# Performance work log

Hardware: AMD Instinct MI355X
Metric: run time of the kernel (lower is better)

The kernel has to match this reference:

```python
import jax, jax.numpy as jnp
import numpy as np

PARENTS = np.array([-1, 0, 1, 1, 1])
NECK_CHAIN = np.array([1, 0])  # neck joint (1) up to root (0)
B, V, F, J, S, E = 512, 5023, 9976, 5, 100, 50
L_STAT, L_DYN, L_FULL, N_BUCKET = 51, 17, 68, 79


def rodrigues(rvec):
    """Axis-angle [N,3] -> rotation matrices [N,3,3]."""
    angle = jnp.linalg.norm(rvec + 1e-8, axis=-1, keepdims=True)  # [N,1]
    axis = rvec / angle
    s = jnp.sin(angle)[..., None]
    c = jnp.cos(angle)[..., None]
    rx, ry, rz = axis[:, 0], axis[:, 1], axis[:, 2]
    z = jnp.zeros_like(rx)
    K = jnp.stack([z, -rz, ry, rz, z, -rx, -ry, rx, z], axis=-1).reshape(-1, 3, 3)
    I = jnp.eye(3, dtype=rvec.dtype)
    return I + s * K + (1.0 - c) * (K @ K)


def verts2lmk(vertices, faces, lmk_faces_idx, lmk_bary):
    lmk_faces = faces[lmk_faces_idx]                               # [B,L,3]
    lmk_verts = jax.vmap(lambda v, f: v[f])(vertices, lmk_faces)   # [B,L,3verts,3xyz]
    return jnp.einsum('blfc,blf->blc', lmk_verts, lmk_bary)


def setup_inputs() -> dict:
    key = jax.random.key(0)
    ks = jax.random.split(key, 16)
    shape_params = jax.random.normal(ks[0], (B, S), jnp.float32)
    expression_params = jax.random.normal(ks[1], (B, E), jnp.float32)
    pose_params = 0.2 * jax.random.normal(ks[2], (B, 6), jnp.float32)
    eye_pose_params = 0.1 * jax.random.normal(ks[3], (B, 6), jnp.float32)
    v_template = jax.random.normal(ks[4], (V, 3), jnp.float32) * 0.1
    shapedirs = jax.random.normal(ks[5], (V, 3, S + E), jnp.float32) * 0.01
    posedirs = jax.random.normal(ks[6], ((J - 1) * 9, V * 3), jnp.float32) * 0.01
    jr = jax.random.uniform(ks[7], (J, V), jnp.float32)
    J_regressor = jr / jnp.sum(jr, axis=1, keepdims=True)
    lbs_weights = jax.nn.softmax(jax.random.normal(ks[8], (V, J), jnp.float32), axis=-1)
    faces = jax.random.randint(ks[9], (F, 3), 0, V)
    lmk_faces_idx = jax.random.randint(ks[10], (L_STAT,), 0, F)
    lb = jax.random.uniform(ks[11], (L_STAT, 3), jnp.float32) + 1e-3
    lmk_bary_coords = lb / jnp.sum(lb, axis=-1, keepdims=True)
    dynamic_lmk_faces_idx = jax.random.randint(ks[12], (N_BUCKET, L_DYN), 0, F)
    db = jax.random.uniform(ks[13], (N_BUCKET, L_DYN, 3), jnp.float32) + 1e-3
    dynamic_lmk_bary_coords = db / jnp.sum(db, axis=-1, keepdims=True)
    full_lmk_faces_idx = jax.random.randint(ks[14], (L_FULL,), 0, F)
    fb = jax.random.uniform(ks[15], (L_FULL, 3), jnp.float32) + 1e-3
    full_lmk_bary_coords = fb / jnp.sum(fb, axis=-1, keepdims=True)
    return {
        'shape_params': shape_params, 'expression_params': expression_params,
        'pose_params': pose_params, 'eye_pose_params': eye_pose_params,
        'v_template': v_template, 'shapedirs': shapedirs, 'posedirs': posedirs,
        'J_regressor': J_regressor, 'lbs_weights': lbs_weights, 'faces': faces,
        'lmk_faces_idx': lmk_faces_idx, 'lmk_bary_coords': lmk_bary_coords,
        'dynamic_lmk_faces_idx': dynamic_lmk_faces_idx,
        'dynamic_lmk_bary_coords': dynamic_lmk_bary_coords,
        'full_lmk_faces_idx': full_lmk_faces_idx,
        'full_lmk_bary_coords': full_lmk_bary_coords,
    }


def reference(shape_params, expression_params, pose_params, eye_pose_params,
              v_template, shapedirs, posedirs, J_regressor, lbs_weights, faces,
              lmk_faces_idx, lmk_bary_coords, dynamic_lmk_faces_idx,
              dynamic_lmk_bary_coords, full_lmk_faces_idx, full_lmk_bary_coords):
    b = shape_params.shape[0]
    nv = v_template.shape[0]
    dt = shape_params.dtype
    betas = jnp.concatenate([shape_params, expression_params], axis=1)          # [B,150]
    neck = jnp.zeros((b, 3), dtype=dt)
    full_pose = jnp.concatenate(
        [pose_params[:, :3], neck, pose_params[:, 3:], eye_pose_params], axis=1)  # [B,15]
    # shape + expression blendshapes
    v_shaped = v_template[None] + jnp.einsum('bl,vcl->bvc', betas, shapedirs)   # [B,V,3]
    joints = jnp.einsum('jv,bvc->bjc', J_regressor, v_shaped)                   # [B,5,3]
    rot_mats = rodrigues(full_pose.reshape(-1, 3)).reshape(b, J, 3, 3)          # [B,5,3,3]
    I3 = jnp.eye(3, dtype=dt)
    pose_feature = (rot_mats[:, 1:] - I3).reshape(b, -1)                        # [B,36]
    v_posed = v_shaped + (pose_feature @ posedirs).reshape(b, nv, 3)
    # kinematic chain -> global joint transforms
    rel_J = joints.at[:, 1:].add(-joints[:, PARENTS[1:]])
    tm = jnp.zeros((b, J, 4, 4), dtype=dt)
    tm = tm.at[:, :, :3, :3].set(rot_mats).at[:, :, :3, 3].set(rel_J).at[:, :, 3, 3].set(1.0)
    chain = [tm[:, 0]]
    for i in range(1, J):
        chain.append(chain[PARENTS[i]] @ tm[:, i])
    A = jnp.stack(chain, axis=1)                                                # [B,5,4,4]
    Rj = jnp.einsum('bjmn,bjn->bjm', A[:, :, :3, :3], joints)
    A_rel = A.at[:, :, :3, 3].add(-Rj)
    # per-vertex skinning
    T = jnp.einsum('vj,bjmn->bvmn', lbs_weights, A_rel)                         # [B,V,4,4]
    vertices = jnp.einsum('bvmn,bvn->bvm', T[:, :, :3, :3], v_posed) + T[:, :, :3, 3]
    # dynamic contour landmark selection from neck kin-chain relative rotation
    aa = full_pose.reshape(b, J, 3)[:, NECK_CHAIN]                              # [B,2,3]
    rc = rodrigues(aa.reshape(-1, 3)).reshape(b, len(NECK_CHAIN), 3, 3)
    rel_rot = jnp.broadcast_to(I3, (b, 3, 3))
    for idx in range(len(NECK_CHAIN)):
        rel_rot = rc[:, idx] @ rel_rot
    sy = jnp.sqrt(rel_rot[:, 0, 0] ** 2 + rel_rot[:, 1, 0] ** 2)
    y_deg = jnp.arctan2(-rel_rot[:, 2, 0], sy) * (180.0 / np.pi)
    y_rot = jnp.round(jnp.minimum(y_deg, 39.0)).astype(jnp.int32)
    neg_mask = y_rot < 0
    big_neg = y_rot < -39
    neg_vals = jnp.where(big_neg, 78, 39 - y_rot)
    y_rot = jnp.where(neg_mask, neg_vals, y_rot)                                # [B] in [0,79)
    dyn_faces = dynamic_lmk_faces_idx[y_rot]                                    # [B,17]
    dyn_bary = dynamic_lmk_bary_coords[y_rot]                                   # [B,17,3]
    lf = jnp.concatenate([dyn_faces, jnp.broadcast_to(lmk_faces_idx[None], (b, lmk_faces_idx.shape[0]))], axis=1)
    lb = jnp.concatenate([dyn_bary, jnp.broadcast_to(lmk_bary_coords[None], (b,) + lmk_bary_coords.shape)], axis=1)
    landmarks2d = verts2lmk(vertices, faces, lf, lb)
    ff = jnp.broadcast_to(full_lmk_faces_idx[None], (b, full_lmk_faces_idx.shape[0]))
    fb = jnp.broadcast_to(full_lmk_bary_coords[None], (b,) + full_lmk_bary_coords.shape)
    landmarks3d = verts2lmk(vertices, faces, ff, fb)
    return (vertices, landmarks2d, landmarks3d)
```

## Files before the change

kernel.cpp:

```cpp
#include <hip/hip_runtime.h>
#include <cstddef>
#include <cstdint>

#define cB   512
#define cV   5023
#define cS   100
#define cE   50
#define cJ   5
#define cLD  17
#define cLF  68

#define cV3    15069
#define cNPAD  15072
#define cKPAD  192

#define OUT_V  ((size_t)cB * cV * 3)
#define OUT_L  ((size_t)cB * cLF * 3)

#define WS_BTN   ((size_t)0)
#define WS_ATM   (WS_BTN + (size_t)cNPAD * 96)
#define WS_JS2   (WS_ATM + (size_t)cB * 96)
#define WS_AREL  (WS_JS2 + 2432)
#define WS_PF    (WS_AREL + (size_t)cB * 60)
#define WS_YROT  (WS_PF + (size_t)cB * 36)

typedef __attribute__((ext_vector_type(8))) short short8;
typedef __attribute__((ext_vector_type(4))) float f32x4;

__device__ __forceinline__ unsigned short f2bf(float x) {
  unsigned int u = __float_as_uint(x);
  u = (u + 0x7fffu + ((u >> 16) & 1u)) >> 16;
  return (unsigned short)u;
}

__device__ __forceinline__ void rodrigues9(float rx, float ry, float rz, float* R) {
  float a0 = rx + 1e-8f, a1 = ry + 1e-8f, a2 = rz + 1e-8f;
  float angle = sqrtf(a0 * a0 + a1 * a1 + a2 * a2);
  float inv = 1.0f / angle;
  float x = rx * inv, y = ry * inv, z = rz * inv;
  float s = sinf(angle), c = cosf(angle);
  float t = 1.0f - c;
  float xy = x * y, xz = x * z, yz = y * z;
  R[0] = 1.0f - t * (y * y + z * z);
  R[1] = -s * z + t * xy;
  R[2] =  s * y + t * xz;
  R[3] =  s * z + t * xy;
  R[4] = 1.0f - t * (x * x + z * z);
  R[5] = -s * x + t * yz;
  R[6] = -s * y + t * xz;
  R[7] =  s * x + t * yz;
  R[8] = 1.0f - t * (x * x + y * y);
}

__global__ void k_js(const float* __restrict__ jreg, const float* __restrict__ sd,
                     const float* __restrict__ vt, float* __restrict__ JSpart) {
  int t = threadIdx.x;
  if (t >= 453) return;
  int c = t / 151, l = t - c * 151;
  int v0 = blockIdx.x * 32;
  int v1 = v0 + 32; if (v1 > cV) v1 = cV;
  float acc[5] = {0.f, 0.f, 0.f, 0.f, 0.f};
#pragma unroll 8
  for (int v = v0; v < v1; ++v) {
    float x = (l < 150) ? sd[(size_t)(v * 3 + c) * 150 + l] : vt[v * 3 + c];
#pragma unroll
    for (int j = 0; j < 5; ++j)
      acc[j] = fmaf(jreg[j * cV + v], x, acc[j]);
  }
#pragma unroll
  for (int j = 0; j < 5; ++j)
    JSpart[(size_t)blockIdx.x * 2272 + (j * 3 + c) * 151 + l] = acc[j];
}

__global__ void k_jsred(const float* __restrict__ JSpart, float* __restrict__ JS2) {
  int e = blockIdx.x * 256 + threadIdx.x;
  if (e >= 2265) return;
  float s = 0.f;
#pragma unroll 8
  for (int p = 0; p < 157; ++p)
    s += JSpart[(size_t)p * 2272 + e];
  int jc = e / 151, l = e - jc * 151;
  JS2[l * 16 + jc] = s;
}

__global__ __launch_bounds__(256) void k_batch(
    const float* __restrict__ shp, const float* __restrict__ expr,
    const float* __restrict__ pose, const float* __restrict__ eyep,
    const float* __restrict__ JS2g, float* __restrict__ Arel,
    float* __restrict__ pf, int* __restrict__ yrot) {
  __shared__ float js2[151 * 16];
  __shared__ float sb[64 * 153];
  const int t = threadIdx.x;
  const int b0 = blockIdx.x * 64;
  for (int i = t; i < 151 * 16; i += 256) js2[i] = JS2g[i];
  for (int e = t; e < 6400; e += 256) {
    int bl = e / 100, l = e - bl * 100;
    sb[bl * 153 + l] = shp[(size_t)(b0 + bl) * 100 + l];
  }
  for (int e = t; e < 3200; e += 256) {
    int bl = e / 50, l = e - bl * 50;
    sb[bl * 153 + 100 + l] = expr[(size_t)(b0 + bl) * 50 + l];
  }
  __syncthreads();
  if (t >= 64) return;
  int b = b0 + t;
  float jnt[5][3];
  {
    const f32x4* J4 = (const f32x4*)(js2 + 150 * 16);
    f32x4 A = J4[0], Bq = J4[1], Cq = J4[2], Dq = J4[3];
    jnt[0][0] = A.x;  jnt[0][1] = A.y;  jnt[0][2] = A.z;
    jnt[1][0] = A.w;  jnt[1][1] = Bq.x; jnt[1][2] = Bq.y;
    jnt[2][0] = Bq.z; jnt[2][1] = Bq.w; jnt[2][2] = Cq.x;
    jnt[3][0] = Cq.y; jnt[3][1] = Cq.z; jnt[3][2] = Cq.w;
    jnt[4][0] = Dq.x; jnt[4][1] = Dq.y; jnt[4][2] = Dq.z;
  }
  for (int l = 0; l < 150; ++l) {
    const f32x4* J4 = (const f32x4*)(js2 + l * 16);
    f32x4 A = J4[0], Bq = J4[1], Cq = J4[2], Dq = J4[3];
    float beta = sb[t * 153 + l];
    jnt[0][0] = fmaf(beta, A.x,  jnt[0][0]);
    jnt[0][1] = fmaf(beta, A.y,  jnt[0][1]);
    jnt[0][2] = fmaf(beta, A.z,  jnt[0][2]);
    jnt[1][0] = fmaf(beta, A.w,  jnt[1][0]);
    jnt[1][1] = fmaf(beta, Bq.x, jnt[1][1]);
    jnt[1][2] = fmaf(beta, Bq.y, jnt[1][2]);
    jnt[2][0] = fmaf(beta, Bq.z, jnt[2][0]);
    jnt[2][1] = fmaf(beta, Bq.w, jnt[2][1]);
    jnt[2][2] = fmaf(beta, Cq.x, jnt[2][2]);
    jnt[3][0] = fmaf(beta, Cq.y, jnt[3][0]);
    jnt[3][1] = fmaf(beta, Cq.z, jnt[3][1]);
    jnt[3][2] = fmaf(beta, Cq.w, jnt[3][2]);
    jnt[4][0] = fmaf(beta, Dq.x, jnt[4][0]);
    jnt[4][1] = fmaf(beta, Dq.y, jnt[4][1]);
    jnt[4][2] = fmaf(beta, Dq.z, jnt[4][2]);
  }
  float fp[5][3];
  fp[0][0] = pose[b * 6 + 0]; fp[0][1] = pose[b * 6 + 1]; fp[0][2] = pose[b * 6 + 2];
  fp[1][0] = 0.f; fp[1][1] = 0.f; fp[1][2] = 0.f;
  fp[2][0] = pose[b * 6 + 3]; fp[2][1] = pose[b * 6 + 4]; fp[2][2] = pose[b * 6 + 5];
  fp[3][0] = eyep[b * 6 + 0]; fp[3][1] = eyep[b * 6 + 1]; fp[3][2] = eyep[b * 6 + 2];
  fp[4][0] = eyep[b * 6 + 3]; fp[4][1] = eyep[b * 6 + 4]; fp[4][2] = eyep[b * 6 + 5];
  float R[5][9];
#pragma unroll
  for (int j = 0; j < 5; ++j) rodrigues9(fp[j][0], fp[j][1], fp[j][2], R[j]);
#pragma unroll
  for (int j = 1; j < 5; ++j)
#pragma unroll
    for (int r = 0; r < 9; ++r) {
      float id = (r == 0 || r == 4 || r == 8) ? 1.f : 0.f;
      pf[b * 36 + (j - 1) * 9 + r] = R[j][r] - id;
    }
  float rel[5][3];
#pragma unroll
  for (int c = 0; c < 3; ++c) {
    rel[0][c] = jnt[0][c];
    rel[1][c] = jnt[1][c] - jnt[0][c];
    rel[2][c] = jnt[2][c] - jnt[1][c];
    rel[3][c] = jnt[3][c] - jnt[1][c];
    rel[4][c] = jnt[4][c] - jnt[1][c];
  }
  float GR[5][9], Gt[5][3];
#pragma unroll
  for (int r = 0; r < 9; ++r) GR[0][r] = R[0][r];
#pragma unroll
  for (int c = 0; c < 3; ++c) Gt[0][c] = rel[0][c];
  const int par[5] = {0, 0, 1, 1, 1};
#pragma unroll
  for (int j = 1; j < 5; ++j) {
    int p = par[j];
#pragma unroll
    for (int r = 0; r < 3; ++r) {
#pragma unroll
      for (int cc = 0; cc < 3; ++cc)
        GR[j][r * 3 + cc] = GR[p][r * 3 + 0] * R[j][0 + cc] +
                            GR[p][r * 3 + 1] * R[j][3 + cc] +
                            GR[p][r * 3 + 2] * R[j][6 + cc];
      Gt[j][r] = Gt[p][r] + GR[p][r * 3 + 0] * rel[j][0] +
                            GR[p][r * 3 + 1] * rel[j][1] +
                            GR[p][r * 3 + 2] * rel[j][2];
    }
  }
#pragma unroll
  for (int j = 0; j < 5; ++j)
#pragma unroll
    for (int r = 0; r < 3; ++r) {
      float tj = Gt[j][r] - (GR[j][r * 3 + 0] * jnt[j][0] +
                             GR[j][r * 3 + 1] * jnt[j][1] +
                             GR[j][r * 3 + 2] * jnt[j][2]);
      Arel[b * 60 + j * 12 + r * 4 + 0] = GR[j][r * 3 + 0];
      Arel[b * 60 + j * 12 + r * 4 + 1] = GR[j][r * 3 + 1];
      Arel[b * 60 + j * 12 + r * 4 + 2] = GR[j][r * 3 + 2];
      Arel[b * 60 + j * 12 + r * 4 + 3] = tj;
    }
  float Ra[9], Rb[9];
  rodrigues9(fp[1][0], fp[1][1], fp[1][2], Ra);
  rodrigues9(fp[0][0], fp[0][1], fp[0][2], Rb);
  float r00 = Rb[0] * Ra[0] + Rb[1] * Ra[3] + Rb[2] * Ra[6];
  float r10 = Rb[3] * Ra[0] + Rb[4] * Ra[3] + Rb[5] * Ra[6];
  float r20 = Rb[6] * Ra[0] + Rb[7] * Ra[3] + Rb[8] * Ra[6];
  float sy = sqrtf(r00 * r00 + r10 * r10);
  float ydeg = atan2f(-r20, sy) * 57.29577951308232f;
  int y = (int)rintf(fminf(ydeg, 39.0f));
  if (y < 0) y = (y < -39) ? 78 : (39 - y);
  yrot[b] = y;
}

#define QB ((size_t)cNPAD * 48)
__global__ void k_prep(const float* __restrict__ sd, const float* __restrict__ shp,
                       const float* __restrict__ expr, const float* __restrict__ pfm,
                       unsigned int* __restrict__ btn_u2, unsigned int* __restrict__ atm_u2) {
  size_t idx = (size_t)blockIdx.x * 256 + threadIdx.x;
  unsigned short o[4];
  if (idx < QB) {
    int n = (int)(idx / 48), kq = (int)(idx - (size_t)n * 48);
#pragma unroll
    for (int j = 0; j < 4; ++j) {
      int k = kq * 4 + j;
      float v = (n < cV3 && k < 150) ? sd[(size_t)n * 150 + k] : 0.f;
      o[j] = f2bf(v);
    }
    btn_u2[idx * 2 + 0] = (unsigned int)o[0] | ((unsigned int)o[1] << 16);
    btn_u2[idx * 2 + 1] = (unsigned int)o[2] | ((unsigned int)o[3] << 16);
  } else {
    size_t r = idx - QB;
    int m = (int)(r / 48), kq = (int)(r - (size_t)m * 48);
#pragma unroll
    for (int j = 0; j < 4; ++j) {
      int k = kq * 4 + j;
      float v;
      if (k < cS)            v = shp[m * cS + k];
      else if (k < 150)      v = expr[m * cE + (k - cS)];
      else if (k < 186)      v = pfm[m * 36 + (k - 150)];
      else                   v = 0.f;
      o[j] = f2bf(v);
    }
    atm_u2[r * 2 + 0] = (unsigned int)o[0] | ((unsigned int)o[1] << 16);
    atm_u2[r * 2 + 1] = (unsigned int)o[2] | ((unsigned int)o[3] << 16);
  }
}

__global__ void k_pdT(const float* __restrict__ pd, unsigned int* __restrict__ btn_u) {
  __shared__ unsigned short T[64 * 36];
  const int t = threadIdx.x;
  const int n0 = blockIdx.x * 64;
#pragma unroll
  for (int it = 0; it < 9; ++it) {
    int e = t + it * 256;
    int kk = e >> 6, ln = e & 63;
    int n = n0 + ln;
    float v = (n < cV3) ? pd[(size_t)kk * cV3 + n] : 0.f;
    T[ln * 36 + kk] = f2bf(v);
  }
  __syncthreads();
  for (int e = t; e < 64 * 18; e += 256) {
    int ln = e / 18, d = e - ln * 18;
    int n = n0 + ln;
    if (n < cV3) {
      unsigned int w = (unsigned int)T[ln * 36 + 2 * d] |
                       ((unsigned int)T[ln * 36 + 2 * d + 1] << 16);
      btn_u[(size_t)n * 96 + 75 + d] = w;
    }
  }
}

__global__ __launch_bounds__(256) void k_main(
    const unsigned short* __restrict__ BTn, const unsigned short* __restrict__ ATm,
    const float* __restrict__ Arel, const float* __restrict__ vtempl,
    const float* __restrict__ lbw, float* __restrict__ out) {
  __shared__ __align__(16) unsigned short smem[19200];
  float* Pf = (float*)smem;

  const int bid = blockIdx.x;
  const int r8 = bid & 7, q = bid >> 3;
  const int mb = q & 7, nbh = q >> 3;
  const int nb = (nbh << 3) | r8;
  if (nb >= 157) return;

  const int t = threadIdx.x;
  const int w = t >> 6, L = t & 63;
  const int wm = w >> 1, wn = w & 1;
  const int lr = L & 15, lq = L >> 4;

  const unsigned short* bsrc = BTn + (size_t)nb * 96 * 192;
  uint4 bst[9];
#pragma unroll
  for (int it = 0; it < 9; ++it)
    bst[it] = *(const uint4*)(bsrc + ((size_t)(t + it * 256)) * 8);
#pragma unroll
  for (int it = 0; it < 9; ++it) {
    int e = t + it * 256;
    int row = e / 24, col = e - row * 24;
    *(uint4*)(smem + row * 200 + col * 8) = bst[it];
  }
  __syncthreads();

  f32x4 acc[2][3];
#pragma unroll
  for (int mt = 0; mt < 2; ++mt)
#pragma unroll
    for (int nt = 0; nt < 3; ++nt) acc[mt][nt] = (f32x4){0.f, 0.f, 0.f, 0.f};

  const unsigned short* abase = ATm + ((size_t)mb * 64 + wm * 32 + lr) * 192 + lq * 8;
#pragma unroll
  for (int ks = 0; ks < 6; ++ks) {
    short8 af0 = *(const short8*)(abase + ks * 32);
    short8 af1 = *(const short8*)(abase + 16 * 192 + ks * 32);
    const int ko = ks * 32 + lq * 8;
    short8 bf[3];
#pragma unroll
    for (int nt = 0; nt < 3; ++nt)
      bf[nt] = *(const short8*)(smem + (wn * 48 + nt * 16 + lr) * 200 + ko);
#pragma unroll
    for (int nt = 0; nt < 3; ++nt) {
      acc[0][nt] = __builtin_amdgcn_mfma_f32_16x16x32_bf16(af0, bf[nt], acc[0][nt], 0, 0, 0);
      acc[1][nt] = __builtin_amdgcn_mfma_f32_16x16x32_bf16(af1, bf[nt], acc[1][nt], 0, 0, 0);
    }
  }
  __syncthreads();

#pragma unroll
  for (int mt = 0; mt < 2; ++mt)
#pragma unroll
    for (int nt = 0; nt < 3; ++nt) {
      int m_base = wm * 32 + mt * 16 + lq * 4;
      int n_loc  = wn * 48 + nt * 16 + lr;
      *(f32x4*)(Pf + n_loc * 68 + m_base) = acc[mt][nt];
    }
  __syncthreads();

  const int v_loc = t & 31, bgrp = t >> 5;
  const int v = nb * 32 + v_loc;
  float wj[5], vtl[3];
  const bool vok = (v < cV);
#pragma unroll
  for (int j = 0; j < 5; ++j) wj[j] = vok ? lbw[v * 5 + j] : 0.f;
#pragma unroll
  for (int c = 0; c < 3; ++c) vtl[c] = vok ? vtempl[v * 3 + c] : 0.f;

#pragma unroll
  for (int i = 0; i < 8; ++i) {
    const int b_loc = bgrp * 8 + i;
    const float* qb = Arel + ((size_t)mb * 64 + b_loc) * 60;
    float px = Pf[(v_loc * 3 + 0) * 68 + b_loc] + vtl[0];
    float py = Pf[(v_loc * 3 + 1) * 68 + b_loc] + vtl[1];
    float pz = Pf[(v_loc * 3 + 2) * 68 + b_loc] + vtl[2];
    float o0 = 0.f, o1 = 0.f, o2 = 0.f;
#pragma unroll
    for (int j = 0; j < 5; ++j) {
      f32x4 q0 = *(const f32x4*)(qb + j * 12);
      f32x4 q1 = *(const f32x4*)(qb + j * 12 + 4);
      f32x4 q2 = *(const f32x4*)(qb + j * 12 + 8);
      float s0 = q0.x * px + q0.y * py + q0.z * pz + q0.w;
      float s1 = q1.x * px + q1.y * py + q1.z * pz + q1.w;
      float s2 = q2.x * px + q2.y * py + q2.z * pz + q2.w;
      o0 = fmaf(wj[j], s0, o0);
      o1 = fmaf(wj[j], s1, o1);
      o2 = fmaf(wj[j], s2, o2);
    }
    if (vok) {
      const int b = mb * 64 + b_loc;
      size_t off = ((size_t)b * cV + v) * 3;
      out[off + 0] = o0;
      out[off + 1] = o1;
      out[off + 2] = o2;
    }
  }
}

__global__ void k_lmk(const float* __restrict__ verts, const int* __restrict__ faces,
                      const int* __restrict__ lmkf, const float* __restrict__ lmkb,
                      const int* __restrict__ dynf, const float* __restrict__ dynb,
                      const int* __restrict__ fullf, const float* __restrict__ fullb,
                      const int* __restrict__ yrot, float* __restrict__ out) {
  int id = blockIdx.x * 256 + threadIdx.x;
  if (id >= cB * cLF * 2) return;
  int sel = id & 1;
  int r = id >> 1;
  int b = r / cLF, l = r - b * cLF;
  const float* vb = verts + (size_t)b * cV * 3;
  int f; float w0, w1, w2; size_t o;
  if (sel == 0) {
    if (l < cLD) {
      int yb = yrot[b];
      f = dynf[yb * cLD + l];
      const float* bp = dynb + ((size_t)yb * cLD + l) * 3;
      w0 = bp[0]; w1 = bp[1]; w2 = bp[2];
    } else {
      f = lmkf[l - cLD];
      const float* bp = lmkb + (size_t)(l - cLD) * 3;
      w0 = bp[0]; w1 = bp[1]; w2 = bp[2];
    }
    o = OUT_V + ((size_t)b * cLF + l) * 3;
  } else {
    f = fullf[l];
    const float* bp = fullb + (size_t)l * 3;
    w0 = bp[0]; w1 = bp[1]; w2 = bp[2];
    o = OUT_V + OUT_L + ((size_t)b * cLF + l) * 3;
  }
  int i0 = faces[f * 3 + 0] * 3, i1 = faces[f * 3 + 1] * 3, i2 = faces[f * 3 + 2] * 3;
  out[o + 0] = w0 * vb[i0 + 0] + w1 * vb[i1 + 0] + w2 * vb[i2 + 0];
  out[o + 1] = w0 * vb[i0 + 1] + w1 * vb[i1 + 1] + w2 * vb[i2 + 1];
  out[o + 2] = w0 * vb[i0 + 2] + w1 * vb[i1 + 2] + w2 * vb[i2 + 2];
}

extern "C" void kernel_launch(void* const* d_in, const int* in_sizes, int n_in,
                              void* d_out, int out_size, void* d_ws, size_t ws_size,
                              hipStream_t stream) {
  (void)in_sizes; (void)n_in; (void)out_size; (void)ws_size;
  const float* shp  = (const float*)d_in[0];
  const float* expr = (const float*)d_in[1];
  const float* pose = (const float*)d_in[2];
  const float* eyep = (const float*)d_in[3];
  const float* vt   = (const float*)d_in[4];
  const float* sd   = (const float*)d_in[5];
  const float* pd   = (const float*)d_in[6];
  const float* jreg = (const float*)d_in[7];
  const float* lbw  = (const float*)d_in[8];
  const int*   fcs  = (const int*)d_in[9];
  const int*   lmkf = (const int*)d_in[10];
  const float* lmkb = (const float*)d_in[11];
  const int*   dynf = (const int*)d_in[12];
  const float* dynb = (const float*)d_in[13];
  const int*   fullf= (const int*)d_in[14];
  const float* fullb= (const float*)d_in[15];
  float* out = (float*)d_out;
  float* ws  = (float*)d_ws;

  unsigned short* BTn = (unsigned short*)(ws + WS_BTN);
  unsigned short* ATm = (unsigned short*)(ws + WS_ATM);
  float* JSpart = ws + WS_BTN;
  float* JS2  = ws + WS_JS2;
  float* Arel = ws + WS_AREL;
  float* pf   = ws + WS_PF;
  int*   yrot = (int*)(ws + WS_YROT);

  k_js<<<157, 512, 0, stream>>>(jreg, sd, vt, JSpart);
  k_jsred<<<9, 256, 0, stream>>>(JSpart, JS2);
  k_batch<<<8, 256, 0, stream>>>(shp, expr, pose, eyep, JS2, Arel, pf, yrot);
  k_prep<<<2922, 256, 0, stream>>>(sd, shp, expr, pf,
                                   (unsigned int*)BTn, (unsigned int*)ATm);
  k_pdT<<<236, 256, 0, stream>>>(pd, (unsigned int*)BTn);
  k_main<<<1280, 256, 0, stream>>>(BTn, ATm, Arel, vt, lbw, out);
  k_lmk<<<272, 256, 0, stream>>>(out, fcs, lmkf, lmkb, dynf, dynb, fullf, fullb, yrot, out);
}
```

Baseline: 186.5 us.

## Fuse shapedir/posedir bf16 packing with joint regression and batch prep

Merges the joint-shape regression, the shapedir bf16 conversion and the posedir transpose into one kernel that stages each 96-row slab of shapedirs in shared memory. Both the packing and the J_regressor reduction then read from that one staged copy. The A-matrix packing moves into k_batch, which now runs 16 blocks of 32 and keeps the pose features in shared memory, so two launches and a global pf round-trip disappear. k_main also prefetches the next A fragments one k-step ahead. The cost is a heavier k_dirs with large shared-memory use and fewer, fatter blocks, plus a separate workspace slot for JSpart.

```diff
diff --git a/kernel.cpp b/kernel.cpp
--- a/kernel.cpp
+++ b/kernel.cpp
@@ -12,17 +12,16 @@
 
 #define cV3    15069
 #define cNPAD  15072
-#define cKPAD  192
 
 #define OUT_V  ((size_t)cB * cV * 3)
 #define OUT_L  ((size_t)cB * cLF * 3)
 
-#define WS_BTN   ((size_t)0)
-#define WS_ATM   (WS_BTN + (size_t)cNPAD * 96)
-#define WS_JS2   (WS_ATM + (size_t)cB * 96)
-#define WS_AREL  (WS_JS2 + 2432)
-#define WS_PF    (WS_AREL + (size_t)cB * 60)
-#define WS_YROT  (WS_PF + (size_t)cB * 36)
+#define WS_BTN    ((size_t)0)
+#define WS_ATM    (WS_BTN + (size_t)cNPAD * 96)
+#define WS_JS2    (WS_ATM + (size_t)cB * 96)
+#define WS_AREL   (WS_JS2 + 2432)
+#define WS_YROT   (WS_AREL + (size_t)cB * 60)
+#define WS_JSPART (WS_YROT + 512)
 
 typedef __attribute__((ext_vector_type(8))) short short8;
 typedef __attribute__((ext_vector_type(4))) float f32x4;
@@ -52,24 +51,67 @@
   R[8] = 1.0f - t * (x * x + y * y);
 }
 
-__global__ void k_js(const float* __restrict__ jreg, const float* __restrict__ sd,
-                     const float* __restrict__ vt, float* __restrict__ JSpart) {
-  int t = threadIdx.x;
-  if (t >= 453) return;
-  int c = t / 151, l = t - c * 151;
-  int v0 = blockIdx.x * 32;
-  int v1 = v0 + 32; if (v1 > cV) v1 = cV;
-  float acc[5] = {0.f, 0.f, 0.f, 0.f, 0.f};
+__global__ __launch_bounds__(512) void k_dirs(
+    const float* __restrict__ sd, const float* __restrict__ pd,
+    const float* __restrict__ jreg, const float* __restrict__ vt,
+    unsigned int* __restrict__ btn_u, float* __restrict__ JSpart) {
+  __shared__ float sdt[96 * 152];
+  __shared__ unsigned short pdt[96 * 38];
+  const int t = threadIdx.x;
+  const int nb = blockIdx.x;
+  const int n0 = nb * 96, v0 = nb * 32;
+
+  const size_t gbase = (size_t)n0 * 150;
+  for (int idx = t; idx < 14400; idx += 512) {
+    size_t g = gbase + idx;
+    float v = (g < (size_t)cV3 * 150) ? sd[g] : 0.f;
+    int row = idx / 150, col = idx - row * 150;
+    sdt[row * 152 + col] = v;
+  }
+  for (int e = t; e < 3456; e += 512) {
+    int pdk = e / 96, row = e - pdk * 96;
+    int n = n0 + row;
+    float v = (n < cV3) ? pd[(size_t)pdk * cV3 + n] : 0.f;
+    pdt[row * 38 + pdk] = f2bf(v);
+  }
+  __syncthreads();
+
+#pragma unroll
+  for (int it = 0; it < 18; ++it) {
+    int e = t + it * 512;
+    int row = e / 96, d = e - row * 96;
+    unsigned int wv;
+    if (d < 75) {
+      wv = (unsigned int)f2bf(sdt[row * 152 + 2 * d]) |
+           ((unsigned int)f2bf(sdt[row * 152 + 2 * d + 1]) << 16);
+    } else if (d < 93) {
+      wv = (unsigned int)pdt[row * 38 + (d - 75) * 2] |
+           ((unsigned int)pdt[row * 38 + (d - 75) * 2 + 1] << 16);
+    } else {
+      wv = 0u;
+    }
+    btn_u[(size_t)(n0 + row) * 96 + d] = wv;
+  }
+
+  if (t < 453) {
+    int c = t / 151, l = t - c * 151;
+    float acc[5] = {0.f, 0.f, 0.f, 0.f, 0.f};
 #pragma unroll 8
-  for (int v = v0; v < v1; ++v) {
-    float x = (l < 150) ? sd[(size_t)(v * 3 + c) * 150 + l] : vt[v * 3 + c];
+    for (int v_loc = 0; v_loc < 32; ++v_loc) {
+      int v = v0 + v_loc;
+      bool ok = (v < cV);
+      float x = (l < 150) ? sdt[(v_loc * 3 + c) * 152 + l]
+                          : (ok ? vt[v * 3 + c] : 0.f);
+#pragma unroll
+      for (int j = 0; j < 5; ++j) {
+        float g = ok ? jreg[j * cV + v] : 0.f;
+        acc[j] = fmaf(g, x, acc[j]);
+      }
+    }
 #pragma unroll
     for (int j = 0; j < 5; ++j)
-      acc[j] = fmaf(jreg[j * cV + v], x, acc[j]);
-  }
-#pragma unroll
-  for (int j = 0; j < 5; ++j)
-    JSpart[(size_t)blockIdx.x * 2272 + (j * 3 + c) * 151 + l] = acc[j];
+      JSpart[(size_t)nb * 2272 + (j * 3 + c) * 151 + l] = acc[j];
+  }
 }
 
 __global__ void k_jsred(const float* __restrict__ JSpart, float* __restrict__ JS2) {
@@ -87,179 +129,142 @@
     const float* __restrict__ shp, const float* __restrict__ expr,
     const float* __restrict__ pose, const float* __restrict__ eyep,
     const float* __restrict__ JS2g, float* __restrict__ Arel,
-    float* __restrict__ pf, int* __restrict__ yrot) {
+    int* __restrict__ yrot, unsigned int* __restrict__ atm_u) {
   __shared__ float js2[151 * 16];
-  __shared__ float sb[64 * 153];
+  __shared__ float sb[32 * 153];
+  __shared__ float pfs[32 * 36];
   const int t = threadIdx.x;
-  const int b0 = blockIdx.x * 64;
+  const int b0 = blockIdx.x * 32;
   for (int i = t; i < 151 * 16; i += 256) js2[i] = JS2g[i];
-  for (int e = t; e < 6400; e += 256) {
+  for (int e = t; e < 3200; e += 256) {
     int bl = e / 100, l = e - bl * 100;
     sb[bl * 153 + l] = shp[(size_t)(b0 + bl) * 100 + l];
   }
-  for (int e = t; e < 3200; e += 256) {
+  for (int e = t; e < 1600; e += 256) {
     int bl = e / 50, l = e - bl * 50;
     sb[bl * 153 + 100 + l] = expr[(size_t)(b0 + bl) * 50 + l];
   }
   __syncthreads();
-  if (t >= 64) return;
-  int b = b0 + t;
-  float jnt[5][3];
-  {
-    const f32x4* J4 = (const f32x4*)(js2 + 150 * 16);
-    f32x4 A = J4[0], Bq = J4[1], Cq = J4[2], Dq = J4[3];
-    jnt[0][0] = A.x;  jnt[0][1] = A.y;  jnt[0][2] = A.z;
-    jnt[1][0] = A.w;  jnt[1][1] = Bq.x; jnt[1][2] = Bq.y;
-    jnt[2][0] = Bq.z; jnt[2][1] = Bq.w; jnt[2][2] = Cq.x;
-    jnt[3][0] = Cq.y; jnt[3][1] = Cq.z; jnt[3][2] = Cq.w;
-    jnt[4][0] = Dq.x; jnt[4][1] = Dq.y; jnt[4][2] = Dq.z;
-  }
-  for (int l = 0; l < 150; ++l) {
-    const f32x4* J4 = (const f32x4*)(js2 + l * 16);
-    f32x4 A = J4[0], Bq = J4[1], Cq = J4[2], Dq = J4[3];
-    float beta = sb[t * 153 + l];
-    jnt[0][0] = fmaf(beta, A.x,  jnt[0][0]);
-    jnt[0][1] = fmaf(beta, A.y,  jnt[0][1]);
-    jnt[0][2] = fmaf(beta, A.z,  jnt[0][2]);
-    jnt[1][0] = fmaf(beta, A.w,  jnt[1][0]);
-    jnt[1][1] = fmaf(beta, Bq.x, jnt[1][1]);
-    jnt[1][2] = fmaf(beta, Bq.y, jnt[1][2]);
-    jnt[2][0] = fmaf(beta, Bq.z, jnt[2][0]);
-    jnt[2][1] = fmaf(beta, Bq.w, jnt[2][1]);
-    jnt[2][2] = fmaf(beta, Cq.x, jnt[2][2]);
-    jnt[3][0] = fmaf(beta, Cq.y, jnt[3][0]);
-    jnt[3][1] = fmaf(beta, Cq.z, jnt[3][1]);
-    jnt[3][2] = fmaf(beta, Cq.w, jnt[3][2]);
-    jnt[4][0] = fmaf(beta, Dq.x, jnt[4][0]);
-    jnt[4][1] = fmaf(beta, Dq.y, jnt[4][1]);
-    jnt[4][2] = fmaf(beta, Dq.z, jnt[4][2]);
-  }
-  float fp[5][3];
-  fp[0][0] = pose[b * 6 + 0]; fp[0][1] = pose[b * 6 + 1]; fp[0][2] = pose[b * 6 + 2];
-  fp[1][0] = 0.f; fp[1][1] = 0.f; fp[1][2] = 0.f;
-  fp[2][0] = pose[b * 6 + 3]; fp[2][1] = pose[b * 6 + 4]; fp[2][2] = pose[b * 6 + 5];
-  fp[3][0] = eyep[b * 6 + 0]; fp[3][1] = eyep[b * 6 + 1]; fp[3][2] = eyep[b * 6 + 2];
-  fp[4][0] = eyep[b * 6 + 3]; fp[4][1] = eyep[b * 6 + 4]; fp[4][2] = eyep[b * 6 + 5];
-  float R[5][9];
-#pragma unroll
-  for (int j = 0; j < 5; ++j) rodrigues9(fp[j][0], fp[j][1], fp[j][2], R[j]);
-#pragma unroll
-  for (int j = 1; j < 5; ++j)
-#pragma unroll
-    for (int r = 0; r < 9; ++r) {
-      float id = (r == 0 || r == 4 || r == 8) ? 1.f : 0.f;
-      pf[b * 36 + (j - 1) * 9 + r] = R[j][r] - id;
-    }
-  float rel[5][3];
-#pragma unroll
-  for (int c = 0; c < 3; ++c) {
-    rel[0][c] = jnt[0][c];
-    rel[1][c] = jnt[1][c] - jnt[0][c];
-    rel[2][c] = jnt[2][c] - jnt[1][c];
-    rel[3][c] = jnt[3][c] - jnt[1][c];
-    rel[4][c] = jnt[4][c] - jnt[1][c];
-  }
-  float GR[5][9], Gt[5][3];
-#pragma unroll
-  for (int r = 0; r < 9; ++r) GR[0][r] = R[0][r];
-#pragma unroll
-  for (int c = 0; c < 3; ++c) Gt[0][c] = rel[0][c];
-  const int par[5] = {0, 0, 1, 1, 1};
-#pragma unroll
-  for (int j = 1; j < 5; ++j) {
-    int p = par[j];
-#pragma unroll
-    for (int r = 0; r < 3; ++r) {
-#pragma unroll
-      for (int cc = 0; cc < 3; ++cc)
-        GR[j][r * 3 + cc] = GR[p][r * 3 + 0] * R[j][0 + cc] +
-                            GR[p][r * 3 + 1] * R[j][3 + cc] +
-                            GR[p][r * 3 + 2] * R[j][6 + cc];
-      Gt[j][r] = Gt[p][r] + GR[p][r * 3 + 0] * rel[j][0] +
-                            GR[p][r * 3 + 1] * rel[j][1] +
-                            GR[p][r * 3 + 2] * rel[j][2];
-    }
-  }
-#pragma unroll
-  for (int j = 0; j < 5; ++j)
-#pragma unroll
-    for (int r = 0; r < 3; ++r) {
-      float tj = Gt[j][r] - (GR[j][r * 3 + 0] * jnt[j][0] +
-                             GR[j][r * 3 + 1] * jnt[j][1] +
-                             GR[j][r * 3 + 2] * jnt[j][2]);
-      Arel[b * 60 + j * 12 + r * 4 + 0] = GR[j][r * 3 + 0];
-      Arel[b * 60 + j * 12 + r * 4 + 1] = GR[j][r * 3 + 1];
-      Arel[b * 60 + j * 12 + r * 4 + 2] = GR[j][r * 3 + 2];
-      Arel[b * 60 + j * 12 + r * 4 + 3] = tj;
-    }
-  float Ra[9], Rb[9];
-  rodrigues9(fp[1][0], fp[1][1], fp[1][2], Ra);
-  rodrigues9(fp[0][0], fp[0][1], fp[0][2], Rb);
-  float r00 = Rb[0] * Ra[0] + Rb[1] * Ra[3] + Rb[2] * Ra[6];
-  float r10 = Rb[3] * Ra[0] + Rb[4] * Ra[3] + Rb[5] * Ra[6];
-  float r20 = Rb[6] * Ra[0] + Rb[7] * Ra[3] + Rb[8] * Ra[6];
-  float sy = sqrtf(r00 * r00 + r10 * r10);
-  float ydeg = atan2f(-r20, sy) * 57.29577951308232f;
-  int y = (int)rintf(fminf(ydeg, 39.0f));
-  if (y < 0) y = (y < -39) ? 78 : (39 - y);
-  yrot[b] = y;
-}
-
-#define QB ((size_t)cNPAD * 48)
-__global__ void k_prep(const float* __restrict__ sd, const float* __restrict__ shp,
-                       const float* __restrict__ expr, const float* __restrict__ pfm,
-                       unsigned int* __restrict__ btn_u2, unsigned int* __restrict__ atm_u2) {
-  size_t idx = (size_t)blockIdx.x * 256 + threadIdx.x;
-  unsigned short o[4];
-  if (idx < QB) {
-    int n = (int)(idx / 48), kq = (int)(idx - (size_t)n * 48);
-#pragma unroll
-    for (int j = 0; j < 4; ++j) {
-      int k = kq * 4 + j;
-      float v = (n < cV3 && k < 150) ? sd[(size_t)n * 150 + k] : 0.f;
-      o[j] = f2bf(v);
-    }
-    btn_u2[idx * 2 + 0] = (unsigned int)o[0] | ((unsigned int)o[1] << 16);
-    btn_u2[idx * 2 + 1] = (unsigned int)o[2] | ((unsigned int)o[3] << 16);
-  } else {
-    size_t r = idx - QB;
-    int m = (int)(r / 48), kq = (int)(r - (size_t)m * 48);
-#pragma unroll
-    for (int j = 0; j < 4; ++j) {
-      int k = kq * 4 + j;
-      float v;
-      if (k < cS)            v = shp[m * cS + k];
-      else if (k < 150)      v = expr[m * cE + (k - cS)];
-      else if (k < 186)      v = pfm[m * 36 + (k - 150)];
-      else                   v = 0.f;
-      o[j] = f2bf(v);
-    }
-    atm_u2[r * 2 + 0] = (unsigned int)o[0] | ((unsigned int)o[1] << 16);
-    atm_u2[r * 2 + 1] = (unsigned int)o[2] | ((unsigned int)o[3] << 16);
-  }
-}
-
-__global__ void k_pdT(const float* __restrict__ pd, unsigned int* __restrict__ btn_u) {
-  __shared__ unsigned short T[64 * 36];
-  const int t = threadIdx.x;
-  const int n0 = blockIdx.x * 64;
-#pragma unroll
-  for (int it = 0; it < 9; ++it) {
+
+  if (t < 32) {
+    int b = b0 + t;
+    float jnt[5][3];
+    {
+      const f32x4* J4 = (const f32x4*)(js2 + 150 * 16);
+      f32x4 A = J4[0], Bq = J4[1], Cq = J4[2], Dq = J4[3];
+      jnt[0][0] = A.x;  jnt[0][1] = A.y;  jnt[0][2] = A.z;
+      jnt[1][0] = A.w;  jnt[1][1] = Bq.x; jnt[1][2] = Bq.y;
+      jnt[2][0] = Bq.z; jnt[2][1] = Bq.w; jnt[2][2] = Cq.x;
+      jnt[3][0] = Cq.y; jnt[3][1] = Cq.z; jnt[3][2] = Cq.w;
+      jnt[4][0] = Dq.x; jnt[4][1] = Dq.y; jnt[4][2] = Dq.z;
+    }
+    for (int l = 0; l < 150; ++l) {
+      const f32x4* J4 = (const f32x4*)(js2 + l * 16);
+      f32x4 A = J4[0], Bq = J4[1], Cq = J4[2], Dq = J4[3];
+      float beta = sb[t * 153 + l];
+      jnt[0][0] = fmaf(beta, A.x,  jnt[0][0]);
+      jnt[0][1] = fmaf(beta, A.y,  jnt[0][1]);
+      jnt[0][2] = fmaf(beta, A.z,  jnt[0][2]);
+      jnt[1][0] = fmaf(beta, A.w,  jnt[1][0]);
+      jnt[1][1] = fmaf(beta, Bq.x, jnt[1][1]);
+      jnt[1][2] = fmaf(beta, Bq.y, jnt[1][2]);
+      jnt[2][0] = fmaf(beta, Bq.z, jnt[2][0]);
+      jnt[2][1] = fmaf(beta, Bq.w, jnt[2][1]);
+      jnt[2][2] = fmaf(beta, Cq.x, jnt[2][2]);
+      jnt[3][0] = fmaf(beta, Cq.y, jnt[3][0]);
+      jnt[3][1] = fmaf(beta, Cq.z, jnt[3][1]);
+      jnt[3][2] = fmaf(beta, Cq.w, jnt[3][2]);
+      jnt[4][0] = fmaf(beta, Dq.x, jnt[4][0]);
+      jnt[4][1] = fmaf(beta, Dq.y, jnt[4][1]);
+      jnt[4][2] = fmaf(beta, Dq.z, jnt[4][2]);
+    }
+    float fp[5][3];
+    fp[0][0] = pose[b * 6 + 0]; fp[0][1] = pose[b * 6 + 1]; fp[0][2] = pose[b * 6 + 2];
+    fp[1][0] = 0.f; fp[1][1] = 0.f; fp[1][2] = 0.f;
+    fp[2][0] = pose[b * 6 + 3]; fp[2][1] = pose[b * 6 + 4]; fp[2][2] = pose[b * 6 + 5];
+    fp[3][0] = eyep[b * 6 + 0]; fp[3][1] = eyep[b * 6 + 1]; fp[3][2] = eyep[b * 6 + 2];
+    fp[4][0] = eyep[b * 6 + 3]; fp[4][1] = eyep[b * 6 + 4]; fp[4][2] = eyep[b * 6 + 5];
+    float R[5][9];
+#pragma unroll
+    for (int j = 0; j < 5; ++j) rodrigues9(fp[j][0], fp[j][1], fp[j][2], R[j]);
+#pragma unroll
+    for (int j = 1; j < 5; ++j)
+#pragma unroll
+      for (int r = 0; r < 9; ++r) {
+        float id = (r == 0 || r == 4 || r == 8) ? 1.f : 0.f;
+        pfs[t * 36 + (j - 1) * 9 + r] = R[j][r] - id;
+      }
+    float rel[5][3];
+#pragma unroll
+    for (int c = 0; c < 3; ++c) {
+      rel[0][c] = jnt[0][c];
+      rel[1][c] = jnt[1][c] - jnt[0][c];
+      rel[2][c] = jnt[2][c] - jnt[1][c];
+      rel[3][c] = jnt[3][c] - jnt[1][c];
+      rel[4][c] = jnt[4][c] - jnt[1][c];
+    }
+    float GR[5][9], Gt[5][3];
+#pragma unroll
+    for (int r = 0; r < 9; ++r) GR[0][r] = R[0][r];
+#pragma unroll
+    for (int c = 0; c < 3; ++c) Gt[0][c] = rel[0][c];
+    const int par[5] = {0, 0, 1, 1, 1};
+#pragma unroll
+    for (int j = 1; j < 5; ++j) {
+      int p = par[j];
+#pragma unroll
+      for (int r = 0; r < 3; ++r) {
+#pragma unroll
+        for (int cc = 0; cc < 3; ++cc)
+          GR[j][r * 3 + cc] = GR[p][r * 3 + 0] * R[j][0 + cc] +
+                              GR[p][r * 3 + 1] * R[j][3 + cc] +
+                              GR[p][r * 3 + 2] * R[j][6 + cc];
+        Gt[j][r] = Gt[p][r] + GR[p][r * 3 + 0] * rel[j][0] +
+                              GR[p][r * 3 + 1] * rel[j][1] +
+                              GR[p][r * 3 + 2] * rel[j][2];
+      }
+    }
+#pragma unroll
+    for (int j = 0; j < 5; ++j)
+#pragma unroll
+      for (int r = 0; r < 3; ++r) {
+        float tj = Gt[j][r] - (GR[j][r * 3 + 0] * jnt[j][0] +
+                               GR[j][r * 3 + 1] * jnt[j][1] +
+                               GR[j][r * 3 + 2] * jnt[j][2]);
+        Arel[b * 60 + j * 12 + r * 4 + 0] = GR[j][r * 3 + 0];
+        Arel[b * 60 + j * 12 + r * 4 + 1] = GR[j][r * 3 + 1];
+        Arel[b * 60 + j * 12 + r * 4 + 2] = GR[j][r * 3 + 2];
+        Arel[b * 60 + j * 12 + r * 4 + 3] = tj;
+      }
+    float Ra[9], Rb[9];
+    rodrigues9(fp[1][0], fp[1][1], fp[1][2], Ra);
+    rodrigues9(fp[0][0], fp[0][1], fp[0][2], Rb);
+    float r00 = Rb[0] * Ra[0] + Rb[1] * Ra[3] + Rb[2] * Ra[6];
+    float r10 = Rb[3] * Ra[0] + Rb[4] * Ra[3] + Rb[5] * Ra[6];
+    float r20 = Rb[6] * Ra[0] + Rb[7] * Ra[3] + Rb[8] * Ra[6];
+    float sy = sqrtf(r00 * r00 + r10 * r10);
+    float ydeg = atan2f(-r20, sy) * 57.29577951308232f;
+    int y = (int)rintf(fminf(ydeg, 39.0f));
+    if (y < 0) y = (y < -39) ? 78 : (39 - y);
+    yrot[b] = y;
+  }
+  __syncthreads();
+
+#pragma unroll
+  for (int it = 0; it < 12; ++it) {
     int e = t + it * 256;
-    int kk = e >> 6, ln = e & 63;
-    int n = n0 + ln;
-    float v = (n < cV3) ? pd[(size_t)kk * cV3 + n] : 0.f;
-    T[ln * 36 + kk] = f2bf(v);
-  }
-  __syncthreads();
-  for (int e = t; e < 64 * 18; e += 256) {
-    int ln = e / 18, d = e - ln * 18;
-    int n = n0 + ln;
-    if (n < cV3) {
-      unsigned int w = (unsigned int)T[ln * 36 + 2 * d] |
-                       ((unsigned int)T[ln * 36 + 2 * d + 1] << 16);
-      btn_u[(size_t)n * 96 + 75 + d] = w;
-    }
+    int bl = e / 96, d = e - bl * 96;
+    unsigned int wv;
+    if (d < 75) {
+      wv = (unsigned int)f2bf(sb[bl * 153 + 2 * d]) |
+           ((unsigned int)f2bf(sb[bl * 153 + 2 * d + 1]) << 16);
+    } else if (d < 93) {
+      wv = (unsigned int)f2bf(pfs[bl * 36 + (d - 75) * 2]) |
+           ((unsigned int)f2bf(pfs[bl * 36 + (d - 75) * 2 + 1]) << 16);
+    } else {
+      wv = 0u;
+    }
+    atm_u[(size_t)(b0 + bl) * 96 + d] = wv;
   }
 }
 
@@ -301,10 +306,15 @@
     for (int nt = 0; nt < 3; ++nt) acc[mt][nt] = (f32x4){0.f, 0.f, 0.f, 0.f};
 
   const unsigned short* abase = ATm + ((size_t)mb * 64 + wm * 32 + lr) * 192 + lq * 8;
+  short8 af0 = *(const short8*)(abase);
+  short8 af1 = *(const short8*)(abase + 16 * 192);
 #pragma unroll
   for (int ks = 0; ks < 6; ++ks) {
-    short8 af0 = *(const short8*)(abase + ks * 32);
-    short8 af1 = *(const short8*)(abase + 16 * 192 + ks * 32);
+    short8 nf0, nf1;
+    if (ks < 5) {
+      nf0 = *(const short8*)(abase + (ks + 1) * 32);
+      nf1 = *(const short8*)(abase + 16 * 192 + (ks + 1) * 32);
+    }
     const int ko = ks * 32 + lq * 8;
     short8 bf[3];
 #pragma unroll
@@ -315,6 +325,7 @@
       acc[0][nt] = __builtin_amdgcn_mfma_f32_16x16x32_bf16(af0, bf[nt], acc[0][nt], 0, 0, 0);
       acc[1][nt] = __builtin_amdgcn_mfma_f32_16x16x32_bf16(af1, bf[nt], acc[1][nt], 0, 0, 0);
     }
+    af0 = nf0; af1 = nf1;
   }
   __syncthreads();
 
@@ -428,18 +439,15 @@
 
   unsigned short* BTn = (unsigned short*)(ws + WS_BTN);
   unsigned short* ATm = (unsigned short*)(ws + WS_ATM);
-  float* JSpart = ws + WS_BTN;
-  float* JS2  = ws + WS_JS2;
-  float* Arel = ws + WS_AREL;
-  float* pf   = ws + WS_PF;
-  int*   yrot = (int*)(ws + WS_YROT);
-
-  k_js<<<157, 512, 0, stream>>>(jreg, sd, vt, JSpart);
+  float* JS2    = ws + WS_JS2;
+  float* Arel   = ws + WS_AREL;
+  int*   yrot   = (int*)(ws + WS_YROT);
+  float* JSpart = ws + WS_JSPART;
+
+  k_dirs<<<157, 512, 0, stream>>>(sd, pd, jreg, vt, (unsigned int*)BTn, JSpart);
   k_jsred<<<9, 256, 0, stream>>>(JSpart, JS2);
-  k_batch<<<8, 256, 0, stream>>>(shp, expr, pose, eyep, JS2, Arel, pf, yrot);
-  k_prep<<<2922, 256, 0, stream>>>(sd, shp, expr, pf,
-                                   (unsigned int*)BTn, (unsigned int*)ATm);
-  k_pdT<<<236, 256, 0, stream>>>(pd, (unsigned int*)BTn);
+  k_batch<<<16, 256, 0, stream>>>(shp, expr, pose, eyep, JS2, Arel, yrot,
+                                  (unsigned int*)ATm);
   k_main<<<1280, 256, 0, stream>>>(BTn, ATm, Arel, vt, lbw, out);
   k_lmk<<<272, 256, 0, stream>>>(out, fcs, lmkf, lmkb, dynf, dynb, fullf, fullb, yrot, out);
 }
```

After: 195.1 us. +4.6%, slower.
